# Kernel optimization log

Measured on AMD Instinct MI355X. Metric: run time of the kernel, lower is better.

Reference implementation:

```python
import jax, jax.numpy as jnp
import numpy as np

L, N, C = 128, 32, 128
DIM_MLP, OUT = 128, 128


def setup_inputs() -> dict:
    key = jax.random.key(0)
    ks = jax.random.split(key, 6)
    s_in2 = 1.0 / np.sqrt(2 * C)
    s_mid = 1.0 / np.sqrt(DIM_MLP)
    s_in = 1.0 / np.sqrt(C)
    return {
        "x": jax.random.normal(ks[0], (L, N, C), jnp.float32),
        "attn_w1": jax.random.normal(ks[1], (2 * C, DIM_MLP), jnp.float32) * s_in2,
        "attn_b1": jnp.zeros((DIM_MLP,), jnp.float32),
        "attn_w2": jax.random.normal(ks[2], (DIM_MLP, OUT), jnp.float32) * s_mid,
        "attn_b2": jnp.zeros((OUT,), jnp.float32),
        "value_w1": jax.random.normal(ks[3], (C, DIM_MLP), jnp.float32) * s_in,
        "value_b1": jnp.zeros((DIM_MLP,), jnp.float32),
        "value_w2": jax.random.normal(ks[4], (DIM_MLP, OUT), jnp.float32) * s_mid,
        "value_b2": jnp.zeros((OUT,), jnp.float32),
    }


def reference(x, attn_w1, attn_b1, attn_w2, attn_b2,
              value_w1, value_b1, value_w2, value_b2):
    l, n, c = x.shape
    # Outer concat: pair[i, j, b] = concat(x[i, b], x[j, b])  -> (l, l, N, 2C)
    xi = jnp.broadcast_to(x[:, None, :, :], (l, l, n, c))
    xj = jnp.broadcast_to(x[None, :, :, :], (l, l, n, c))
    pair = jnp.concatenate([xi, xj], axis=-1)
    # Pairwise attention MLP (ReLU hidden, linear output)
    h = jax.nn.relu(pair @ attn_w1 + attn_b1)          # (l, l, N, dim_mlp)
    attn = h @ attn_w2 + attn_b2                       # (l, l, N, out)
    # Value MLP
    hv = jax.nn.relu(x @ value_w1 + value_b1)          # (l, N, dim_mlp)
    value = hv @ value_w2 + value_b2                   # (l, N, out)
    # Elementwise weighted reduce over key axis j (NOT a matmul over channels)
    out = jnp.einsum('ijbc,jbc->ibc', attn, value)     # (l, N, out)
    return out
```

## Files before the change

### kernel.cpp

```cpp
#include <hip/hip_runtime.h>
#include <hip/hip_bf16.h>

#define L_DIM 128
#define N_DIM 32
#define C_DIM 128
#define K_DIM 128
#define OUT_DIM 128

typedef __attribute__((ext_vector_type(8))) short short8;
typedef __attribute__((ext_vector_type(4))) float float4v;

static __device__ __forceinline__ short bf16_bits(float f) {
    __bf16 h = (__bf16)f;
    return __builtin_bit_cast(short, h);
}

__global__ __launch_bounds__(256) void k_pre(
    const float* __restrict__ x,
    const float* __restrict__ attn_w1, const float* __restrict__ attn_b1,
    const float* __restrict__ attn_w2,
    const float* __restrict__ value_w1, const float* __restrict__ value_b1,
    const float* __restrict__ value_w2, const float* __restrict__ value_b2,
    float* __restrict__ P, float* __restrict__ Q, float* __restrict__ V,
    short* __restrict__ W2s)
{
    int bid = blockIdx.x;
    if (bid >= 512) {
        int e = (bid - 512) * 256 + threadIdx.x;
        int idx  = e & 7;
        int colr = (e >> 3) & 15;
        int quad = (e >> 7) & 3;
        int mi   = (e >> 9) & 3;
        int ct   = e >> 11;
        int k = quad * 8 + 32 * mi + idx;
        int c = ct * 16 + colr;
        W2s[e] = bf16_bits(attn_w2[k * OUT_DIM + c]);
        return;
    }

    __shared__ float xs[8][C_DIM];
    __shared__ float hvs[8][K_DIM];
    int tid = threadIdx.x;
    int r0  = bid * 8;

    {
        int flat = tid * 4;
        int row = flat >> 7, c = flat & 127;
        *(float4v*)(&xs[row][c]) = *(const float4v*)(x + (r0 + row) * C_DIM + c);
    }
    __syncthreads();

    int ks   = tid & 127;
    int half = tid >> 7;

    float pacc[4] = {0,0,0,0}, qacc[4] = {0,0,0,0}, hacc[4] = {0,0,0,0};
    for (int c = 0; c < C_DIM; ++c) {
        float wa = attn_w1[c * K_DIM + ks];
        float wb = attn_w1[(C_DIM + c) * K_DIM + ks];
        float wv = value_w1[c * K_DIM + ks];
        #pragma unroll
        for (int r = 0; r < 4; ++r) {
            float xr = xs[half * 4 + r][c];
            pacc[r] = fmaf(xr, wa, pacc[r]);
            qacc[r] = fmaf(xr, wb, qacc[r]);
            hacc[r] = fmaf(xr, wv, hacc[r]);
        }
    }
    float b1 = attn_b1[ks], vb1 = value_b1[ks];
    #pragma unroll
    for (int r = 0; r < 4; ++r) {
        int rr = r0 + half * 4 + r;
        int i = rr >> 5, b = rr & 31;
        P[(b * L_DIM + i) * K_DIM + ks] = pacc[r];
        Q[(b * L_DIM + i) * K_DIM + ks] = qacc[r] + b1;
        hvs[half * 4 + r][ks] = fmaxf(hacc[r] + vb1, 0.f);
    }
    __syncthreads();

    float vacc[4] = {0,0,0,0};
    for (int k = 0; k < K_DIM; ++k) {
        float w = value_w2[k * OUT_DIM + ks];
        #pragma unroll
        for (int r = 0; r < 4; ++r)
            vacc[r] = fmaf(hvs[half * 4 + r][k], w, vacc[r]);
    }
    float vb2 = value_b2[ks];
    #pragma unroll
    for (int r = 0; r < 4; ++r) {
        int rr = r0 + half * 4 + r;
        int i = rr >> 5, b = rr & 31;
        V[(b * L_DIM + i) * OUT_DIM + ks] = vacc[r] + vb2;
    }
}

__global__ __launch_bounds__(256) void k_sv(const float* __restrict__ V,
                                            float* __restrict__ Sv)
{
    int t = blockIdx.x * 256 + threadIdx.x;
    int b = t >> 7, c = t & 127;
    float s = 0.f;
    for (int j = 0; j < L_DIM; ++j)
        s += V[(b * L_DIM + j) * OUT_DIM + c];
    Sv[t] = s;
}

__global__ __launch_bounds__(256, 2) void k_main(
    const float* __restrict__ P, const float* __restrict__ Q,
    const float* __restrict__ V, const float* __restrict__ Sv,
    const short* __restrict__ W2s, const float* __restrict__ attn_b2,
    float* __restrict__ out)
{
    int b     = blockIdx.x >> 5;
    int itile = blockIdx.x & 31;
    int wave  = threadIdx.x >> 6;
    int lane  = threadIdx.x & 63;
    int i     = itile * 4 + wave;
    int quad  = lane >> 4;
    int col   = lane & 15;

    short8 bfrag[8][4];
    const short8* w2p = (const short8*)W2s;
    #pragma unroll
    for (int ct = 0; ct < 8; ++ct)
        #pragma unroll
        for (int mi = 0; mi < 4; ++mi)
            bfrag[ct][mi] = w2p[((ct * 4 + mi) * 4 + quad) * 16 + col];

    float4v p[4][2];
    const float* Pr = P + (b * L_DIM + i) * K_DIM;
    #pragma unroll
    for (int mi = 0; mi < 4; ++mi) {
        int k0 = quad * 8 + 32 * mi;
        p[mi][0] = *(const float4v*)(Pr + k0);
        p[mi][1] = *(const float4v*)(Pr + k0 + 4);
    }

    float acc[8] = {0,0,0,0,0,0,0,0};

    for (int j0 = 0; j0 < L_DIM; j0 += 16) {
        const float* Qr = Q + (b * L_DIM + j0 + col) * K_DIM;
        short8 af[4];
        #pragma unroll
        for (int mi = 0; mi < 4; ++mi) {
            int k0 = quad * 8 + 32 * mi;
            float4v q0 = *(const float4v*)(Qr + k0);
            float4v q1 = *(const float4v*)(Qr + k0 + 4);
            short8 a;
            #pragma unroll
            for (int t = 0; t < 4; ++t) {
                a[t]     = bf16_bits(fmaxf(p[mi][0][t] + q0[t], 0.f));
                a[t + 4] = bf16_bits(fmaxf(p[mi][1][t] + q1[t], 0.f));
            }
            af[mi] = a;
        }

        const float* Vr = V + (b * L_DIM + j0 + quad * 4) * OUT_DIM;
        #pragma unroll
        for (int ct = 0; ct < 8; ++ct) {
            float4v c = {0.f, 0.f, 0.f, 0.f};
            #pragma unroll
            for (int mi = 0; mi < 4; ++mi)
                c = __builtin_amdgcn_mfma_f32_16x16x32_bf16(af[mi], bfrag[ct][mi], c, 0, 0, 0);
            int cc = ct * 16 + col;
            #pragma unroll
            for (int r = 0; r < 4; ++r)
                acc[ct] = fmaf(c[r], Vr[r * OUT_DIM + cc], acc[ct]);
        }
    }

    #pragma unroll
    for (int ct = 0; ct < 8; ++ct) {
        acc[ct] += __shfl_xor(acc[ct], 16, 64);
        acc[ct] += __shfl_xor(acc[ct], 32, 64);
    }

    if (quad == 0) {
        #pragma unroll
        for (int ct = 0; ct < 8; ++ct) {
            int cc = ct * 16 + col;
            out[(i * N_DIM + b) * OUT_DIM + cc] =
                acc[ct] + attn_b2[cc] * Sv[b * OUT_DIM + cc];
        }
    }
}

extern "C" void kernel_launch(void* const* d_in, const int* in_sizes, int n_in,
                              void* d_out, int out_size, void* d_ws, size_t ws_size,
                              hipStream_t stream)
{
    const float* x        = (const float*)d_in[0];
    const float* attn_w1  = (const float*)d_in[1];
    const float* attn_b1  = (const float*)d_in[2];
    const float* attn_w2  = (const float*)d_in[3];
    const float* attn_b2  = (const float*)d_in[4];
    const float* value_w1 = (const float*)d_in[5];
    const float* value_b1 = (const float*)d_in[6];
    const float* value_w2 = (const float*)d_in[7];
    const float* value_b2 = (const float*)d_in[8];
    float* out = (float*)d_out;

    float* ws  = (float*)d_ws;
    float* P   = ws;
    float* Q   = ws + 524288;
    float* V   = ws + 1048576;
    float* Sv  = ws + 1572864;
    short* W2s = (short*)(ws + 1576960);

    k_pre<<<576, 256, 0, stream>>>(x, attn_w1, attn_b1, attn_w2,
                                   value_w1, value_b1, value_w2, value_b2,
                                   P, Q, V, W2s);
    k_sv<<<16, 256, 0, stream>>>(V, Sv);
    k_main<<<1024, 256, 0, stream>>>(P, Q, V, Sv, W2s, attn_b2, out);
}
```

Measured before the change: 138.6 us.

## Stage Q/V tiles in LDS with double buffering and cooperative A-fragment build

The main kernel now double-buffers Q and V tiles in LDS through a software-pipelined loop. All 256 threads cooperatively build the bf16 ReLU(P+Q) A-fragments into a swizzled LDS buffer once per block, instead of each wave reading global Q and V with strided per-lane loads. The pre-kernel is split into twice as many smaller blocks with unroll hints, and the column-sum kernel is parallelised over more blocks with a shared-memory reduction. The change adds barriers and LDS pressure in exchange for less redundant global traffic and better load coalescing.

```diff
diff --git a/kernel.cpp b/kernel.cpp
--- a/kernel.cpp
+++ b/kernel.cpp
@@ -9,6 +9,7 @@
 
 typedef __attribute__((ext_vector_type(8))) short short8;
 typedef __attribute__((ext_vector_type(4))) float float4v;
+typedef __attribute__((ext_vector_type(2))) float float2v;
 
 static __device__ __forceinline__ short bf16_bits(float f) {
     __bf16 h = (__bf16)f;
@@ -25,8 +26,8 @@
     short* __restrict__ W2s)
 {
     int bid = blockIdx.x;
-    if (bid >= 512) {
-        int e = (bid - 512) * 256 + threadIdx.x;
+    if (bid >= 1024) {
+        int e = (bid - 1024) * 256 + threadIdx.x;
         int idx  = e & 7;
         int colr = (e >> 3) & 15;
         int quad = (e >> 7) & 3;
@@ -38,29 +39,30 @@
         return;
     }
 
-    __shared__ float xs[8][C_DIM];
-    __shared__ float hvs[8][K_DIM];
+    __shared__ float xs[4][C_DIM];
+    __shared__ float hvs[4][K_DIM];
     int tid = threadIdx.x;
-    int r0  = bid * 8;
+    int r0  = bid * 4;
 
     {
-        int flat = tid * 4;
-        int row = flat >> 7, c = flat & 127;
-        *(float4v*)(&xs[row][c]) = *(const float4v*)(x + (r0 + row) * C_DIM + c);
+        int f = tid * 2;
+        int row = f >> 7, c = f & 127;
+        *(float2v*)(&xs[row][c]) = *(const float2v*)(x + (r0 + row) * C_DIM + c);
     }
     __syncthreads();
 
     int ks   = tid & 127;
     int half = tid >> 7;
 
-    float pacc[4] = {0,0,0,0}, qacc[4] = {0,0,0,0}, hacc[4] = {0,0,0,0};
+    float pacc[2] = {0,0}, qacc[2] = {0,0}, hacc[2] = {0,0};
+    #pragma unroll 4
     for (int c = 0; c < C_DIM; ++c) {
         float wa = attn_w1[c * K_DIM + ks];
         float wb = attn_w1[(C_DIM + c) * K_DIM + ks];
         float wv = value_w1[c * K_DIM + ks];
         #pragma unroll
-        for (int r = 0; r < 4; ++r) {
-            float xr = xs[half * 4 + r][c];
+        for (int r = 0; r < 2; ++r) {
+            float xr = xs[half * 2 + r][c];
             pacc[r] = fmaf(xr, wa, pacc[r]);
             qacc[r] = fmaf(xr, wb, qacc[r]);
             hacc[r] = fmaf(xr, wv, hacc[r]);
@@ -68,26 +70,27 @@
     }
     float b1 = attn_b1[ks], vb1 = value_b1[ks];
     #pragma unroll
-    for (int r = 0; r < 4; ++r) {
-        int rr = r0 + half * 4 + r;
+    for (int r = 0; r < 2; ++r) {
+        int rr = r0 + half * 2 + r;
         int i = rr >> 5, b = rr & 31;
         P[(b * L_DIM + i) * K_DIM + ks] = pacc[r];
         Q[(b * L_DIM + i) * K_DIM + ks] = qacc[r] + b1;
-        hvs[half * 4 + r][ks] = fmaxf(hacc[r] + vb1, 0.f);
-    }
-    __syncthreads();
-
-    float vacc[4] = {0,0,0,0};
+        hvs[half * 2 + r][ks] = fmaxf(hacc[r] + vb1, 0.f);
+    }
+    __syncthreads();
+
+    float vacc[2] = {0,0};
+    #pragma unroll 4
     for (int k = 0; k < K_DIM; ++k) {
         float w = value_w2[k * OUT_DIM + ks];
         #pragma unroll
-        for (int r = 0; r < 4; ++r)
-            vacc[r] = fmaf(hvs[half * 4 + r][k], w, vacc[r]);
+        for (int r = 0; r < 2; ++r)
+            vacc[r] = fmaf(hvs[half * 2 + r][k], w, vacc[r]);
     }
     float vb2 = value_b2[ks];
     #pragma unroll
-    for (int r = 0; r < 4; ++r) {
-        int rr = r0 + half * 4 + r;
+    for (int r = 0; r < 2; ++r) {
+        int rr = r0 + half * 2 + r;
         int i = rr >> 5, b = rr & 31;
         V[(b * L_DIM + i) * OUT_DIM + ks] = vacc[r] + vb2;
     }
@@ -96,27 +99,42 @@
 __global__ __launch_bounds__(256) void k_sv(const float* __restrict__ V,
                                             float* __restrict__ Sv)
 {
-    int t = blockIdx.x * 256 + threadIdx.x;
-    int b = t >> 7, c = t & 127;
+    __shared__ float red[256];
+    int b = blockIdx.x;
+    int tid = threadIdx.x;
+    int c = tid & 127, jh = tid >> 7;
     float s = 0.f;
-    for (int j = 0; j < L_DIM; ++j)
-        s += V[(b * L_DIM + j) * OUT_DIM + c];
-    Sv[t] = s;
-}
-
-__global__ __launch_bounds__(256, 2) void k_main(
+    #pragma unroll 4
+    for (int jj = 0; jj < 64; ++jj)
+        s += V[(b * L_DIM + jh * 64 + jj) * OUT_DIM + c];
+    red[tid] = s;
+    __syncthreads();
+    if (tid < 128)
+        Sv[b * OUT_DIM + tid] = red[tid] + red[128 + tid];
+}
+
+#define QV_STRIDE 132
+
+__global__ __launch_bounds__(256)
+__attribute__((amdgpu_waves_per_eu(2, 2)))
+void k_main(
     const float* __restrict__ P, const float* __restrict__ Q,
     const float* __restrict__ V, const float* __restrict__ Sv,
     const short* __restrict__ W2s, const float* __restrict__ attn_b2,
     float* __restrict__ out)
 {
+    __shared__ short A_lds[4 * 256 * 8];
+    __shared__ float QV_lds[2][2][16 * QV_STRIDE];
+    __shared__ float P_lds[4 * K_DIM];
+
     int b     = blockIdx.x >> 5;
     int itile = blockIdx.x & 31;
-    int wave  = threadIdx.x >> 6;
-    int lane  = threadIdx.x & 63;
-    int i     = itile * 4 + wave;
+    int tid   = threadIdx.x;
+    int wave  = tid >> 6;
+    int lane  = tid & 63;
     int quad  = lane >> 4;
     int col   = lane & 15;
+    int i_g   = itile * 4 + wave;
 
     short8 bfrag[8][4];
     const short8* w2p = (const short8*)W2s;
@@ -126,46 +144,97 @@
         for (int mi = 0; mi < 4; ++mi)
             bfrag[ct][mi] = w2p[((ct * 4 + mi) * 4 + quad) * 16 + col];
 
-    float4v p[4][2];
-    const float* Pr = P + (b * L_DIM + i) * K_DIM;
-    #pragma unroll
-    for (int mi = 0; mi < 4; ++mi) {
-        int k0 = quad * 8 + 32 * mi;
-        p[mi][0] = *(const float4v*)(Pr + k0);
-        p[mi][1] = *(const float4v*)(Pr + k0 + 4);
-    }
+    {
+        int f = tid * 2;
+        int ii = f >> 7, k = f & 127;
+        *(float2v*)&P_lds[f] =
+            *(const float2v*)(P + (b * L_DIM + itile * 4 + ii) * K_DIM + k);
+    }
+
+    int srow = tid >> 4;
+    int sc8  = (tid & 15) * 8;
+    const float* Qbase = Q + (size_t)(b * L_DIM) * K_DIM;
+    const float* Vbase = V + (size_t)(b * L_DIM) * OUT_DIM;
+
+    {
+        const float* qp = Qbase + (0 * 16 + srow) * K_DIM + sc8;
+        const float* vp = Vbase + (0 * 16 + srow) * OUT_DIM + sc8;
+        float4v qa = *(const float4v*)qp, qb = *(const float4v*)(qp + 4);
+        float4v va = *(const float4v*)vp, vb = *(const float4v*)(vp + 4);
+        *(float4v*)&QV_lds[0][0][srow * QV_STRIDE + sc8]     = qa;
+        *(float4v*)&QV_lds[0][0][srow * QV_STRIDE + sc8 + 4] = qb;
+        *(float4v*)&QV_lds[0][1][srow * QV_STRIDE + sc8]     = va;
+        *(float4v*)&QV_lds[0][1][srow * QV_STRIDE + sc8 + 4] = vb;
+    }
+    __syncthreads();
 
     float acc[8] = {0,0,0,0,0,0,0,0};
-
-    for (int j0 = 0; j0 < L_DIM; j0 += 16) {
-        const float* Qr = Q + (b * L_DIM + j0 + col) * K_DIM;
+    int cur = 0;
+
+    int m_  = tid >> 4;
+    int kq_ = tid & 15;
+
+    for (int r = 0; r < 8; ++r) {
+        {
+            const float* Qc = &QV_lds[cur][0][m_ * QV_STRIDE + kq_ * 8];
+            float4v qa = *(const float4v*)Qc;
+            float4v qb = *(const float4v*)(Qc + 4);
+            #pragma unroll
+            for (int i = 0; i < 4; ++i) {
+                float4v pa = *(const float4v*)&P_lds[i * K_DIM + kq_ * 8];
+                float4v pb = *(const float4v*)&P_lds[i * K_DIM + kq_ * 8 + 4];
+                short8 a;
+                #pragma unroll
+                for (int t = 0; t < 4; ++t) {
+                    a[t]     = bf16_bits(fmaxf(pa[t] + qa[t], 0.f));
+                    a[t + 4] = bf16_bits(fmaxf(pb[t] + qb[t], 0.f));
+                }
+                *(short8*)&A_lds[(i * 256 + kq_ * 16 + (m_ ^ kq_)) * 8] = a;
+            }
+        }
+
+        float4v nqa, nqb, nva, nvb;
+        if (r < 7) {
+            const float* qp = Qbase + ((r + 1) * 16 + srow) * K_DIM + sc8;
+            const float* vp = Vbase + ((r + 1) * 16 + srow) * OUT_DIM + sc8;
+            nqa = *(const float4v*)qp; nqb = *(const float4v*)(qp + 4);
+            nva = *(const float4v*)vp; nvb = *(const float4v*)(vp + 4);
+        }
+
+        __syncthreads();
+
+        int nxt = cur ^ 1;
+        if (r < 7) {
+            *(float4v*)&QV_lds[nxt][0][srow * QV_STRIDE + sc8]     = nqa;
+            *(float4v*)&QV_lds[nxt][0][srow * QV_STRIDE + sc8 + 4] = nqb;
+            *(float4v*)&QV_lds[nxt][1][srow * QV_STRIDE + sc8]     = nva;
+            *(float4v*)&QV_lds[nxt][1][srow * QV_STRIDE + sc8 + 4] = nvb;
+        }
+
         short8 af[4];
         #pragma unroll
-        for (int mi = 0; mi < 4; ++mi) {
-            int k0 = quad * 8 + 32 * mi;
-            float4v q0 = *(const float4v*)(Qr + k0);
-            float4v q1 = *(const float4v*)(Qr + k0 + 4);
-            short8 a;
+        for (int ks = 0; ks < 4; ++ks) {
+            int kq = ks * 4 + quad;
+            af[ks] = *(const short8*)
+                &A_lds[(wave * 256 + kq * 16 + (col ^ kq)) * 8];
+        }
+        const float* Vc = &QV_lds[cur][1][0];
+        #pragma unroll
+        for (int ct = 0; ct < 8; ++ct) {
+            float4v c4 = {0.f, 0.f, 0.f, 0.f};
             #pragma unroll
-            for (int t = 0; t < 4; ++t) {
-                a[t]     = bf16_bits(fmaxf(p[mi][0][t] + q0[t], 0.f));
-                a[t + 4] = bf16_bits(fmaxf(p[mi][1][t] + q1[t], 0.f));
-            }
-            af[mi] = a;
-        }
-
-        const float* Vr = V + (b * L_DIM + j0 + quad * 4) * OUT_DIM;
-        #pragma unroll
-        for (int ct = 0; ct < 8; ++ct) {
-            float4v c = {0.f, 0.f, 0.f, 0.f};
-            #pragma unroll
-            for (int mi = 0; mi < 4; ++mi)
-                c = __builtin_amdgcn_mfma_f32_16x16x32_bf16(af[mi], bfrag[ct][mi], c, 0, 0, 0);
+            for (int ks = 0; ks < 4; ++ks)
+                c4 = __builtin_amdgcn_mfma_f32_16x16x32_bf16(
+                        af[ks], bfrag[ct][ks], c4, 0, 0, 0);
             int cc = ct * 16 + col;
             #pragma unroll
-            for (int r = 0; r < 4; ++r)
-                acc[ct] = fmaf(c[r], Vr[r * OUT_DIM + cc], acc[ct]);
-        }
+            for (int rr = 0; rr < 4; ++rr)
+                acc[ct] = fmaf(c4[rr], Vc[(quad * 4 + rr) * QV_STRIDE + cc],
+                               acc[ct]);
+        }
+
+        __syncthreads();
+        cur ^= 1;
     }
 
     #pragma unroll
@@ -178,7 +247,7 @@
         #pragma unroll
         for (int ct = 0; ct < 8; ++ct) {
             int cc = ct * 16 + col;
-            out[(i * N_DIM + b) * OUT_DIM + cc] =
+            out[(i_g * N_DIM + b) * OUT_DIM + cc] =
                 acc[ct] + attn_b2[cc] * Sv[b * OUT_DIM + cc];
         }
     }
@@ -206,9 +275,9 @@
     float* Sv  = ws + 1572864;
     short* W2s = (short*)(ws + 1576960);
 
-    k_pre<<<576, 256, 0, stream>>>(x, attn_w1, attn_b1, attn_w2,
-                                   value_w1, value_b1, value_w2, value_b2,
-                                   P, Q, V, W2s);
-    k_sv<<<16, 256, 0, stream>>>(V, Sv);
+    k_pre<<<1088, 256, 0, stream>>>(x, attn_w1, attn_b1, attn_w2,
+                                    value_w1, value_b1, value_w2, value_b2,
+                                    P, Q, V, W2s);
+    k_sv<<<32, 256, 0, stream>>>(V, Sv);
     k_main<<<1024, 256, 0, stream>>>(P, Q, V, Sv, W2s, attn_b2, out);
 }
```

Result: faster. 129.8 us (-6.3%).

## Stage Q tiles in double-buffered LDS, fuse V column sum into main kernel

Applied to the files above, without the earlier changes.

The main kernel now cooperatively loads each 16-row Q tile into a padded, double-buffered shared-memory buffer and prefetches the next tile while computing the current one. It also preloads the V values for the tile and accumulates the per-column V sum inline, which removes the separate k_sv launch and its workspace buffer. The pre-kernel loops get partial unrolling. These changes trade extra LDS use, a barrier per iteration and more registers against fewer redundant global Q loads and one fewer kernel launch.

```diff
diff --git a/kernel.cpp b/kernel.cpp
--- a/kernel.cpp
+++ b/kernel.cpp
@@ -9,6 +9,7 @@
 
 typedef __attribute__((ext_vector_type(8))) short short8;
 typedef __attribute__((ext_vector_type(4))) float float4v;
+typedef __attribute__((ext_vector_type(2))) float float2v;
 
 static __device__ __forceinline__ short bf16_bits(float f) {
     __bf16 h = (__bf16)f;
@@ -25,8 +26,9 @@
     short* __restrict__ W2s)
 {
     int bid = blockIdx.x;
+    int tid = threadIdx.x;
     if (bid >= 512) {
-        int e = (bid - 512) * 256 + threadIdx.x;
+        int e = (bid - 512) * 256 + tid;
         int idx  = e & 7;
         int colr = (e >> 3) & 15;
         int quad = (e >> 7) & 3;
@@ -40,12 +42,11 @@
 
     __shared__ float xs[8][C_DIM];
     __shared__ float hvs[8][K_DIM];
-    int tid = threadIdx.x;
-    int r0  = bid * 8;
+    int r0 = bid * 8;
 
     {
-        int flat = tid * 4;
-        int row = flat >> 7, c = flat & 127;
+        int f = tid * 4;
+        int row = f >> 7, c = f & 127;
         *(float4v*)(&xs[row][c]) = *(const float4v*)(x + (r0 + row) * C_DIM + c);
     }
     __syncthreads();
@@ -54,6 +55,7 @@
     int half = tid >> 7;
 
     float pacc[4] = {0,0,0,0}, qacc[4] = {0,0,0,0}, hacc[4] = {0,0,0,0};
+    #pragma unroll 4
     for (int c = 0; c < C_DIM; ++c) {
         float wa = attn_w1[c * K_DIM + ks];
         float wb = attn_w1[(C_DIM + c) * K_DIM + ks];
@@ -78,6 +80,7 @@
     __syncthreads();
 
     float vacc[4] = {0,0,0,0};
+    #pragma unroll 4
     for (int k = 0; k < K_DIM; ++k) {
         float w = value_w2[k * OUT_DIM + ks];
         #pragma unroll
@@ -93,30 +96,26 @@
     }
 }
 
-__global__ __launch_bounds__(256) void k_sv(const float* __restrict__ V,
-                                            float* __restrict__ Sv)
-{
-    int t = blockIdx.x * 256 + threadIdx.x;
-    int b = t >> 7, c = t & 127;
-    float s = 0.f;
-    for (int j = 0; j < L_DIM; ++j)
-        s += V[(b * L_DIM + j) * OUT_DIM + c];
-    Sv[t] = s;
-}
-
-__global__ __launch_bounds__(256, 2) void k_main(
+#define QSTR 132
+
+__global__ __launch_bounds__(256)
+__attribute__((amdgpu_waves_per_eu(2, 2)))
+void k_main(
     const float* __restrict__ P, const float* __restrict__ Q,
-    const float* __restrict__ V, const float* __restrict__ Sv,
+    const float* __restrict__ V,
     const short* __restrict__ W2s, const float* __restrict__ attn_b2,
     float* __restrict__ out)
 {
+    __shared__ float Qb[2][16 * QSTR];
+
     int b     = blockIdx.x >> 5;
     int itile = blockIdx.x & 31;
-    int wave  = threadIdx.x >> 6;
-    int lane  = threadIdx.x & 63;
-    int i     = itile * 4 + wave;
+    int tid   = threadIdx.x;
+    int wave  = tid >> 6;
+    int lane  = tid & 63;
     int quad  = lane >> 4;
     int col   = lane & 15;
+    int i_g   = itile * 4 + wave;
 
     short8 bfrag[8][4];
     const short8* w2p = (const short8*)W2s;
@@ -127,7 +126,7 @@
             bfrag[ct][mi] = w2p[((ct * 4 + mi) * 4 + quad) * 16 + col];
 
     float4v p[4][2];
-    const float* Pr = P + (b * L_DIM + i) * K_DIM;
+    const float* Pr = P + (b * L_DIM + i_g) * K_DIM;
     #pragma unroll
     for (int mi = 0; mi < 4; ++mi) {
         int k0 = quad * 8 + 32 * mi;
@@ -135,16 +134,45 @@
         p[mi][1] = *(const float4v*)(Pr + k0 + 4);
     }
 
+    int srow = tid >> 5;
+    int sc4  = (tid & 31) * 4;
+    const float* Qbase = Q + (size_t)(b * L_DIM) * K_DIM;
+    const float* Vbase = V + (size_t)(b * L_DIM) * OUT_DIM;
+
+    *(float4v*)&Qb[0][srow * QSTR + sc4] =
+        *(const float4v*)(Qbase + srow * K_DIM + sc4);
+    *(float4v*)&Qb[0][(srow + 8) * QSTR + sc4] =
+        *(const float4v*)(Qbase + (srow + 8) * K_DIM + sc4);
+    __syncthreads();
+
     float acc[8] = {0,0,0,0,0,0,0,0};
-
-    for (int j0 = 0; j0 < L_DIM; j0 += 16) {
-        const float* Qr = Q + (b * L_DIM + j0 + col) * K_DIM;
+    float sv[8]  = {0,0,0,0,0,0,0,0};
+
+    #pragma unroll 2
+    for (int r = 0; r < 8; ++r) {
+        int cur = r & 1;
+
+        float4v nq0, nq1;
+        if (r < 7) {
+            const float* qp = Qbase + (r + 1) * 16 * K_DIM;
+            nq0 = *(const float4v*)(qp + srow * K_DIM + sc4);
+            nq1 = *(const float4v*)(qp + (srow + 8) * K_DIM + sc4);
+        }
+
+        const float* Vr = Vbase + (r * 16 + quad * 4) * OUT_DIM + col;
+        float vv[32];
+        #pragma unroll
+        for (int rr = 0; rr < 4; ++rr)
+            #pragma unroll
+            for (int ct = 0; ct < 8; ++ct)
+                vv[rr * 8 + ct] = Vr[rr * OUT_DIM + ct * 16];
+
         short8 af[4];
         #pragma unroll
         for (int mi = 0; mi < 4; ++mi) {
-            int k0 = quad * 8 + 32 * mi;
-            float4v q0 = *(const float4v*)(Qr + k0);
-            float4v q1 = *(const float4v*)(Qr + k0 + 4);
+            const float* qc = &Qb[cur][col * QSTR + quad * 8 + mi * 32];
+            float4v q0 = *(const float4v*)qc;
+            float4v q1 = *(const float4v*)(qc + 4);
             short8 a;
             #pragma unroll
             for (int t = 0; t < 4; ++t) {
@@ -154,33 +182,40 @@
             af[mi] = a;
         }
 
-        const float* Vr = V + (b * L_DIM + j0 + quad * 4) * OUT_DIM;
         #pragma unroll
         for (int ct = 0; ct < 8; ++ct) {
-            float4v c = {0.f, 0.f, 0.f, 0.f};
+            float4v c4 = {0.f, 0.f, 0.f, 0.f};
             #pragma unroll
             for (int mi = 0; mi < 4; ++mi)
-                c = __builtin_amdgcn_mfma_f32_16x16x32_bf16(af[mi], bfrag[ct][mi], c, 0, 0, 0);
-            int cc = ct * 16 + col;
-            #pragma unroll
-            for (int r = 0; r < 4; ++r)
-                acc[ct] = fmaf(c[r], Vr[r * OUT_DIM + cc], acc[ct]);
-        }
+                c4 = __builtin_amdgcn_mfma_f32_16x16x32_bf16(
+                        af[mi], bfrag[ct][mi], c4, 0, 0, 0);
+            #pragma unroll
+            for (int rr = 0; rr < 4; ++rr) {
+                float v = vv[rr * 8 + ct];
+                acc[ct] = fmaf(c4[rr], v, acc[ct]);
+                sv[ct] += v;
+            }
+        }
+
+        if (r < 7) {
+            *(float4v*)&Qb[cur ^ 1][srow * QSTR + sc4]       = nq0;
+            *(float4v*)&Qb[cur ^ 1][(srow + 8) * QSTR + sc4] = nq1;
+        }
+        __syncthreads();
     }
 
     #pragma unroll
     for (int ct = 0; ct < 8; ++ct) {
-        acc[ct] += __shfl_xor(acc[ct], 16, 64);
-        acc[ct] += __shfl_xor(acc[ct], 32, 64);
+        float fin = fmaf(attn_b2[ct * 16 + col], sv[ct], acc[ct]);
+        fin += __shfl_xor(fin, 16, 64);
+        fin += __shfl_xor(fin, 32, 64);
+        acc[ct] = fin;
     }
 
     if (quad == 0) {
         #pragma unroll
-        for (int ct = 0; ct < 8; ++ct) {
-            int cc = ct * 16 + col;
-            out[(i * N_DIM + b) * OUT_DIM + cc] =
-                acc[ct] + attn_b2[cc] * Sv[b * OUT_DIM + cc];
-        }
+        for (int ct = 0; ct < 8; ++ct)
+            out[(i_g * N_DIM + b) * OUT_DIM + ct * 16 + col] = acc[ct];
     }
 }
 
@@ -203,12 +238,10 @@
     float* P   = ws;
     float* Q   = ws + 524288;
     float* V   = ws + 1048576;
-    float* Sv  = ws + 1572864;
-    short* W2s = (short*)(ws + 1576960);
+    short* W2s = (short*)(ws + 1572864);
 
     k_pre<<<576, 256, 0, stream>>>(x, attn_w1, attn_b1, attn_w2,
                                    value_w1, value_b1, value_w2, value_b2,
                                    P, Q, V, W2s);
-    k_sv<<<16, 256, 0, stream>>>(V, Sv);
-    k_main<<<1024, 256, 0, stream>>>(P, Q, V, Sv, W2s, attn_b2, out);
-}
+    k_main<<<1024, 256, 0, stream>>>(P, Q, V, W2s, attn_b2, out);
+}
```

After: 223.7 us. +61.4%, slower.
